# Performance work log

Hardware: AMD Instinct MI355X
Metric: run time of the kernel (lower is better)

The kernel has to match this reference:

```python
import jax, jax.numpy as jnp
import numpy as np

SHUFFLE_G = 8
NUM_HEADS = 8
EPS = 1e-12


def setup_inputs() -> dict:
    key = jax.random.key(0)
    ks = jax.random.split(key, 7)
    b, dim, t, h, w = 2, 64, 10, 128, 128
    c3 = dim * 3
    return {
        "x": jax.random.normal(ks[0], (b, dim, t, h, w), jnp.float32),
        "W1": jax.random.normal(ks[1], (c3, dim), jnp.float32) * 0.05,            # 1x1x1 conv
        "Wdw": jax.random.normal(ks[2], (c3, 1, 1, 3, 3), jnp.float32) * 0.1,     # depthwise (1,3,3) conv
        "W_lin": jax.random.normal(ks[3], (t * SHUFFLE_G, t * SHUFFLE_G), jnp.float32) * 0.05,
        "b_lin": jax.random.normal(ks[4], (t * SHUFFLE_G,), jnp.float32) * 0.01,
        "temperature": jnp.ones((NUM_HEADS, 1, 1), jnp.float32),
        "W_out": jax.random.normal(ks[5], (dim, dim), jnp.float32) * 0.05,        # 1x1x1 conv
    }


def _l2norm(v):
    n = jnp.sqrt(jnp.sum(v * v, axis=-1, keepdims=True))
    return v / jnp.maximum(n, EPS)


def reference(x, W1, Wdw, W_lin, b_lin, temperature, W_out):
    b, c, t, h, w = x.shape
    c3 = 3 * c
    heads = NUM_HEADS
    # 1x1x1 pointwise conv (no bias)
    y = jnp.einsum('oc,bcthw->bothw', W1, x)
    # depthwise (1,3,3) conv, padding (0,1,1)
    y = jax.lax.conv_general_dilated(
        y, Wdw, window_strides=(1, 1, 1),
        padding=((0, 0), (1, 1), (1, 1)),
        dimension_numbers=('NCDHW', 'OIDHW', 'NCDHW'),
        feature_group_count=c3)
    # shuffle: b (c1 c2) t h w -> b c2 h w (c1 t), c1 = SHUFFLE_G
    c1, c2 = SHUFFLE_G, c3 // SHUFFLE_G
    y = y.reshape(b, c1, c2, t, h, w).transpose(0, 2, 4, 5, 1, 3).reshape(b, c2, h, w, c1 * t)
    # linear mixing along (c1 t)
    y = jnp.einsum('bchwi,oi->bchwo', y, W_lin) + b_lin
    # unshuffle: b c2 h w (c1 t) -> b (c2 c1 t) h w
    y = y.reshape(b, c2, h, w, c1, t).transpose(0, 1, 4, 5, 2, 3).reshape(b, c3 * t, h, w)
    # split qkv along channel
    q, k, v = jnp.split(y, 3, axis=1)  # each [b, c*t, h, w]
    ct, hw = (c // heads) * t, h * w
    q = q.reshape(b, heads, ct, hw)
    k = k.reshape(b, heads, ct, hw)
    v = v.reshape(b, heads, ct, hw)
    q = _l2norm(q)
    k = _l2norm(k)
    attn = jnp.einsum('bhcd,bhed->bhce', q, k) * temperature  # [b, heads, ct, ct]
    attn = jax.nn.softmax(attn, axis=-1)
    out = jnp.einsum('bhce,bhed->bhcd', attn, v)  # [b, heads, ct, hw]
    out = out.reshape(b, c, t, h, w)
    out = jnp.einsum('oc,bcthw->bothw', W_out, out)
    return out
```

## Files before the change

### kernel.cpp

```cpp
#include <hip/hip_runtime.h>
#include <hip/hip_bf16.h>

#define C_  64
#define C3_ 192
#define T_  10
#define H_  128
#define W_  128
#define HW_ 16384
#define THW_ 163840
#define NH_ 8
#define C2_ 24
#define TG_ 80

typedef __hip_bfloat16 bf16;
typedef __attribute__((ext_vector_type(8))) short bf16x8;
typedef __attribute__((ext_vector_type(4))) float f32x4;

__device__ __forceinline__ float bf2f(bf16 v) { return __bfloat162float(v); }

__device__ __forceinline__ ushort f2bf_s(float f) {
  bf16 h = __float2bfloat16(f);
  union { bf16 b; ushort s; } u; u.b = h; return u.s;
}

__device__ __forceinline__ ushort4 pack4(f32x4 a) {
  ushort4 p;
  p.x = f2bf_s(a[0]); p.y = f2bf_s(a[1]); p.z = f2bf_s(a[2]); p.w = f2bf_s(a[3]);
  return p;
}

__device__ __forceinline__ uint pack2lo(uint x, uint y) { return (x & 0xffffu) | (y << 16); }
__device__ __forceinline__ uint pack2hi(uint x, uint y) { return (x >> 16) | (y & 0xffff0000u); }

__global__ __launch_bounds__(256) void kprep(
    const float* __restrict__ W1, const float* __restrict__ W_lin,
    const float* __restrict__ W_out,
    bf16* __restrict__ W1bf, bf16* __restrict__ Wlinbf, bf16* __restrict__ Woutbf) {
  const int idx = blockIdx.x * 256 + threadIdx.x;
  if (idx < 12288) {
    W1bf[idx] = __float2bfloat16(W1[idx]);
  } else if (idx < 12288 + 7680) {
    const int i = idx - 12288;
    const int row = i / 96, col = i - row * 96;
    Wlinbf[i] = __float2bfloat16(col < 80 ? W_lin[row * 80 + col] : 0.f);
  } else if (idx < 12288 + 7680 + 4096) {
    const int i = idx - 12288 - 7680;
    Woutbf[i] = __float2bfloat16(W_out[i]);
  }
}

#define K1_TPB 4
__global__ __launch_bounds__(256) void k1_mfma(
    const float* __restrict__ x, const bf16* __restrict__ W1bf,
    bf16* __restrict__ y1ws) {
  __shared__ __align__(16) float xs[2][64 * 128];
  const int tid = threadIdx.x;
  const int lane = tid & 63, wv = tid >> 6;
  const int lr = lane & 15, lg = lane >> 4;
  const int mh = blockIdx.y;
  const int b = blockIdx.z;
  const float* xb = x + (size_t)b * C_ * THW_;
  bf16* y1 = y1ws + (size_t)b * C3_ * THW_;
  const int tile0 = blockIdx.x * K1_TPB;

  const int ro = lane >> 5, colo = (lane & 31) * 4;
  auto STAGE = [&](int buf, int tIdx) {
    const int n0 = tIdx * 128;
#pragma unroll
    for (int i = 0; i < 8; ++i) {
      const int row = wv * 16 + i * 2;
      const float* gsrc = xb + (size_t)(row + ro) * THW_ + n0 + colo;
      __builtin_amdgcn_global_load_lds(
          (const __attribute__((address_space(1))) void*)gsrc,
          (__attribute__((address_space(3))) void*)&xs[buf][row * 128],
          16, 0, 0);
    }
  };

  STAGE(0, tile0);

  bf16x8 wf[6][2];
#pragma unroll
  for (int mt = 0; mt < 6; ++mt)
#pragma unroll
    for (int c = 0; c < 2; ++c) {
      const int row = mh * 96 + mt * 16 + lr;
      wf[mt][c] = *reinterpret_cast<const bf16x8*>(W1bf + row * 64 + c * 32 + lg * 8);
    }
  __syncthreads();

  int buf = 0;
  for (int t = 0; t < K1_TPB; ++t) {
    if (t + 1 < K1_TPB) STAGE(buf ^ 1, tile0 + t + 1);
    const int n0 = (tile0 + t) * 128;
#pragma unroll
    for (int nt = 0; nt < 2; ++nt) {
      const int col = wv * 32 + nt * 16 + lr;
      bf16x8 xa[2];
#pragma unroll
      for (int c = 0; c < 2; ++c) {
        const float* base = &xs[buf][(c * 32 + lg * 8) * 128 + col];
        bf16x8 f;
#pragma unroll
        for (int e = 0; e < 8; ++e) f[e] = f2bf_s(base[e * 128]);
        xa[c] = f;
      }
      f32x4 acc[6];
#pragma unroll
      for (int mt = 0; mt < 6; ++mt) acc[mt] = (f32x4){0.f, 0.f, 0.f, 0.f};
#pragma unroll
      for (int c = 0; c < 2; ++c)
#pragma unroll
        for (int mt = 0; mt < 6; ++mt)
          acc[mt] = __builtin_amdgcn_mfma_f32_16x16x32_bf16(xa[c], wf[mt][c], acc[mt], 0, 0, 0);
      const int nb = n0 + wv * 32 + nt * 16 + lg * 4;
#pragma unroll
      for (int mt = 0; mt < 6; ++mt) {
        const int o = mh * 96 + mt * 16 + lr;
        *reinterpret_cast<ushort4*>(y1 + (size_t)o * THW_ + nb) = pack4(acc[mt]);
      }
    }
    __syncthreads();
    buf ^= 1;
  }
}

__global__ __launch_bounds__(256) void k2_dw(
    const bf16* __restrict__ y1ws, const float* __restrict__ Wdw,
    bf16* __restrict__ y2ws) {
  __shared__ float tile[34][132];
  const int tid = threadIdx.x;
  const int blk = blockIdx.x;
  const int b = blockIdx.y;
  const bf16* y1 = y1ws + (size_t)b * C3_ * THW_;
  bf16* y2 = y2ws + (size_t)b * C3_ * THW_;
  const int hs = (blk & 3) * 32;
  const int rest = blk >> 2;
  const int t = rest % T_;
  const int o = rest / T_;
  const bf16* src = y1 + ((size_t)o * T_ + t) * HW_;

  if (tid < 68) {
    const int r = tid >> 1, side = tid & 1;
    tile[r][side ? 129 : 0] = 0.f;
  }
  {
    const int rr = tid >> 5, c4 = (tid & 31) * 4;
#pragma unroll
    for (int p = 0; p < 5; ++p) {
      const int r = p * 8 + rr;
      if (r < 34) {
        const int hh = hs - 1 + r;
        float e0 = 0.f, e1 = 0.f, e2 = 0.f, e3 = 0.f;
        if (hh >= 0 && hh < H_) {
          uint2 raw = *reinterpret_cast<const uint2*>(src + hh * W_ + c4);
          e0 = __uint_as_float(raw.x << 16);
          e1 = __uint_as_float(raw.x & 0xffff0000u);
          e2 = __uint_as_float(raw.y << 16);
          e3 = __uint_as_float(raw.y & 0xffff0000u);
        }
        tile[r][1 + c4]     = e0;
        tile[r][1 + c4 + 1] = e1;
        tile[r][1 + c4 + 2] = e2;
        tile[r][1 + c4 + 3] = e3;
      }
    }
  }
  __syncthreads();

  float kk[9];
#pragma unroll
  for (int i = 0; i < 9; ++i) kk[i] = Wdw[o * 9 + i];

  bf16* dst = y2 + ((size_t)o * T_ + t) * HW_;
  const int w = tid & 127;
  const int r0 = (tid >> 7) * 16;

  float a[3][3];
#pragma unroll
  for (int ky = 0; ky < 3; ++ky)
#pragma unroll
    for (int kx = 0; kx < 3; ++kx) a[ky][kx] = tile[r0 + ky][w + kx];

#pragma unroll
  for (int q = 0; q < 16; ++q) {
    float acc = 0.f;
#pragma unroll
    for (int ky = 0; ky < 3; ++ky)
#pragma unroll
      for (int kx = 0; kx < 3; ++kx)
        acc = fmaf(kk[ky * 3 + kx], a[ky][kx], acc);
    dst[(hs + r0 + q) * W_ + w] = __float2bfloat16(acc);
    if (q < 15) {
#pragma unroll
      for (int kx = 0; kx < 3; ++kx) {
        a[0][kx] = a[1][kx];
        a[1][kx] = a[2][kx];
        a[2][kx] = tile[r0 + q + 3][w + kx];
      }
    }
  }
}

#define K3_NKC 13
#define K3_STRIDE 208
__global__ __launch_bounds__(256) void k3_mfma(
    const bf16* __restrict__ y2ws, const bf16* __restrict__ Wlinbf,
    const float* __restrict__ b_lin, bf16* __restrict__ zws,
    float* __restrict__ ssqws) {
  __shared__ __align__(16) char lds[256 * K3_STRIDE];
  const int tid = threadIdx.x;
  const int s0 = blockIdx.x * 256;
  const int c2 = blockIdx.y;
  const int b = blockIdx.z;
  const bf16* y2 = y2ws + (size_t)b * C3_ * THW_;
  bf16* z = zws + (size_t)b * C3_ * THW_;
  float* ssq = ssqws + b * 1280;

  {
    auto stage_block = [&](int kc, int cg) {
      uint rr[8][4];
#pragma unroll
      for (int e = 0; e < 8; ++e) {
        const int k = kc * 8 + e;
        const int c1 = (k * 205) >> 11;
        const int tt = k - c1 * 10;
        uint4 raw = *reinterpret_cast<const uint4*>(
            y2 + ((size_t)((c1 * C2_ + c2) * T_ + tt)) * HW_ + s0 + cg * 8);
        rr[e][0] = raw.x; rr[e][1] = raw.y; rr[e][2] = raw.z; rr[e][3] = raw.w;
      }
#pragma unroll
      for (int j = 0; j < 8; ++j) {
        const int d = j >> 1;
        uint4 o;
        if (j & 1) {
          o.x = pack2hi(rr[0][d], rr[1][d]); o.y = pack2hi(rr[2][d], rr[3][d]);
          o.z = pack2hi(rr[4][d], rr[5][d]); o.w = pack2hi(rr[6][d], rr[7][d]);
        } else {
          o.x = pack2lo(rr[0][d], rr[1][d]); o.y = pack2lo(rr[2][d], rr[3][d]);
          o.z = pack2lo(rr[4][d], rr[5][d]); o.w = pack2lo(rr[6][d], rr[7][d]);
        }
        const int col = cg * 8 + j;
        const int r = (kc + col) % K3_NKC;
        *reinterpret_cast<uint4*>(lds + col * K3_STRIDE + r * 16) = o;
      }
    };
    stage_block(tid >> 5, tid & 31);
    if ((tid & 3) == 0) {
      const int q = tid >> 2;
      stage_block(8 + (q >> 5), q & 31);
    }
    const int col = tid;
    const uint4 zero4 = {0, 0, 0, 0};
    *reinterpret_cast<uint4*>(lds + col * K3_STRIDE + ((10 + col) % K3_NKC) * 16) = zero4;
    *reinterpret_cast<uint4*>(lds + col * K3_STRIDE + ((11 + col) % K3_NKC) * 16) = zero4;
  }
  __syncthreads();

  const int lane = tid & 63, wv = tid >> 6;
  const int lr = lane & 15, lg = lane >> 4;

  bf16x8 wf[5][3];
#pragma unroll
  for (int mt = 0; mt < 5; ++mt)
#pragma unroll
    for (int c = 0; c < 3; ++c)
      wf[mt][c] = *reinterpret_cast<const bf16x8*>(
          Wlinbf + (mt * 16 + lr) * 96 + c * 32 + lg * 8);
  float bias[5];
#pragma unroll
  for (int mt = 0; mt < 5; ++mt) bias[mt] = b_lin[mt * 16 + lr];

  float sqp[5] = {0.f, 0.f, 0.f, 0.f, 0.f};

  for (int nt = 0; nt < 4; ++nt) {
    const int col = wv * 64 + nt * 16 + lr;
    bf16x8 xa[3];
#pragma unroll
    for (int c = 0; c < 3; ++c) {
      const int kc = c * 4 + lg;
      xa[c] = *reinterpret_cast<const bf16x8*>(
          lds + col * K3_STRIDE + ((kc + col) % K3_NKC) * 16);
    }
    f32x4 acc[5];
#pragma unroll
    for (int mt = 0; mt < 5; ++mt)
      acc[mt] = (f32x4){bias[mt], bias[mt], bias[mt], bias[mt]};
#pragma unroll
    for (int c = 0; c < 3; ++c)
#pragma unroll
      for (int mt = 0; mt < 5; ++mt)
        acc[mt] = __builtin_amdgcn_mfma_f32_16x16x32_bf16(xa[c], wf[mt][c], acc[mt], 0, 0, 0);
    const int sb = s0 + wv * 64 + nt * 16 + lg * 4;
#pragma unroll
    for (int mt = 0; mt < 5; ++mt) {
      const int u = c2 * TG_ + mt * 16 + lr;
      *reinterpret_cast<ushort4*>(z + (size_t)u * HW_ + sb) = pack4(acc[mt]);
#pragma unroll
      for (int j = 0; j < 4; ++j)
        sqp[mt] = fmaf(acc[mt][j], acc[mt][j], sqp[mt]);
    }
  }

  if (c2 < 16) {
#pragma unroll
    for (int mt = 0; mt < 5; ++mt) {
      float v = sqp[mt];
      v += __shfl_xor(v, 16);
      v += __shfl_xor(v, 32);
      if (lane < 16)
        atomicAdd(&ssq[c2 * TG_ + mt * 16 + lane], v);
    }
  }
}

__global__ __launch_bounds__(256) void k5_mfma(
    const bf16* __restrict__ zws, float* __restrict__ Gpartws) {
  __shared__ __align__(16) float gbuf[2][TG_ * TG_];
  const int chunk = blockIdx.x, h = blockIdx.y, b = blockIdx.z;
  const bf16* z = zws + (size_t)b * C3_ * THW_;
  float* Gpart = Gpartws + (size_t)b * 1638400;
  const int tid = threadIdx.x;
  const int lane = tid & 63, wv = tid >> 6;
  const int lr = lane & 15, lg = lane >> 4;

  const bf16* qbase = z + (size_t)(h * TG_) * HW_;
  const bf16* kbase = z + (size_t)((8 + h) * TG_) * HW_;

  f32x4 acc[5][5];
#pragma unroll
  for (int a = 0; a < 5; ++a)
#pragma unroll
    for (int b2 = 0; b2 < 5; ++b2) acc[a][b2] = (f32x4){0.f, 0.f, 0.f, 0.f};

  const int s0 = chunk * 512 + wv * 128;
  for (int s = s0; s < s0 + 128; s += 32) {
    bf16x8 qa[5], kb[5];
#pragma unroll
    for (int a = 0; a < 5; ++a)
      qa[a] = *reinterpret_cast<const bf16x8*>(qbase + (size_t)(a * 16 + lr) * HW_ + s + lg * 8);
#pragma unroll
    for (int a = 0; a < 5; ++a)
      kb[a] = *reinterpret_cast<const bf16x8*>(kbase + (size_t)(a * 16 + lr) * HW_ + s + lg * 8);
#pragma unroll
    for (int a = 0; a < 5; ++a)
#pragma unroll
      for (int b2 = 0; b2 < 5; ++b2)
        acc[a][b2] = __builtin_amdgcn_mfma_f32_16x16x32_bf16(qa[a], kb[b2], acc[a][b2], 0, 0, 0);
  }

  if (wv == 1 || wv == 3) {
    float* dst = gbuf[wv >> 1];
#pragma unroll
    for (int a = 0; a < 5; ++a)
#pragma unroll
      for (int b2 = 0; b2 < 5; ++b2)
#pragma unroll
        for (int j = 0; j < 4; ++j)
          dst[(a * 16 + lg * 4 + j) * TG_ + b2 * 16 + lr] = acc[a][b2][j];
  }
  __syncthreads();
  if (wv == 0 || wv == 2) {
    const float* srcb = gbuf[wv >> 1];
#pragma unroll
    for (int a = 0; a < 5; ++a)
#pragma unroll
      for (int b2 = 0; b2 < 5; ++b2)
#pragma unroll
        for (int j = 0; j < 4; ++j)
          acc[a][b2][j] += srcb[(a * 16 + lg * 4 + j) * TG_ + b2 * 16 + lr];
  }
  __syncthreads();
  if (wv == 2) {
#pragma unroll
    for (int a = 0; a < 5; ++a)
#pragma unroll
      for (int b2 = 0; b2 < 5; ++b2)
#pragma unroll
        for (int j = 0; j < 4; ++j)
          gbuf[0][(a * 16 + lg * 4 + j) * TG_ + b2 * 16 + lr] = acc[a][b2][j];
  }
  __syncthreads();
  if (wv == 0) {
    float* gp = Gpart + ((size_t)chunk * 8 + h) * TG_ * TG_;
#pragma unroll
    for (int a = 0; a < 5; ++a)
#pragma unroll
      for (int b2 = 0; b2 < 5; ++b2)
#pragma unroll
        for (int j = 0; j < 4; ++j) {
          const int i = a * 16 + lg * 4 + j, jj = b2 * 16 + lr;
          gp[i * TG_ + jj] = acc[a][b2][j] + gbuf[0][i * TG_ + jj];
        }
  }
}

__global__ __launch_bounds__(128) void k6_softmax(
    const float* __restrict__ Gpartws, const float* __restrict__ ssqws,
    const float* __restrict__ temp, bf16* __restrict__ attnbfws) {
  __shared__ float red[128];
  __shared__ float smax, ssum;
  const int b = blockIdx.y;
  const float* Gpart = Gpartws + (size_t)b * 1638400;
  const float* ssq = ssqws + b * 1280;
  bf16* attnbf = attnbfws + (size_t)b * NH_ * TG_ * 96;
  int h = blockIdx.x / TG_, i = blockIdx.x % TG_;
  int j = threadIdx.x;
  float logit = -1e30f;
  if (j < TG_) {
    float g = 0.f;
    for (int c = 0; c < 32; ++c)
      g += Gpart[(((size_t)c * 8 + h) * TG_ + i) * TG_ + j];
    float nq = ssq[h * TG_ + i];
    float nk = ssq[(8 + h) * TG_ + j];
    float sq = 1.f / fmaxf(sqrtf(nq), 1e-12f);
    float sk = 1.f / fmaxf(sqrtf(nk), 1e-12f);
    logit = g * sq * sk * temp[h];
  }
  red[j] = logit;
  __syncthreads();
  if (j == 0) {
    float m = -1e30f;
    for (int x2 = 0; x2 < TG_; ++x2) m = fmaxf(m, red[x2]);
    smax = m;
  }
  __syncthreads();
  float e = (j < TG_) ? expf(logit - smax) : 0.f;
  red[j] = e;
  __syncthreads();
  if (j == 0) {
    float s = 0.f;
    for (int x2 = 0; x2 < TG_; ++x2) s += red[x2];
    ssum = s;
  }
  __syncthreads();
  if (j < 96)
    attnbf[((size_t)h * TG_ + i) * 96 + j] =
        __float2bfloat16(j < TG_ ? e / ssum : 0.f);
}

__global__ __launch_bounds__(256) void k7a_mfma(
    const bf16* __restrict__ zws, const bf16* __restrict__ attnbfws,
    bf16* __restrict__ att_outws) {
  __shared__ __align__(16) char lds[256 * K3_STRIDE];
  const int tid = threadIdx.x;
  const int s0 = blockIdx.x * 256;
  const int h = blockIdx.y;
  const int b = blockIdx.z;
  const bf16* z = zws + (size_t)b * C3_ * THW_;
  const bf16* attnbf = attnbfws + (size_t)b * NH_ * TG_ * 96;
  bf16* att_out = att_outws + (size_t)b * NH_ * TG_ * HW_;
  const int voff = (16 + h) * TG_;

  {
    auto stage_block = [&](int kc, int cg) {
      uint rr[8][4];
#pragma unroll
      for (int e = 0; e < 8; ++e) {
        uint4 raw = *reinterpret_cast<const uint4*>(
            z + (size_t)(voff + kc * 8 + e) * HW_ + s0 + cg * 8);
        rr[e][0] = raw.x; rr[e][1] = raw.y; rr[e][2] = raw.z; rr[e][3] = raw.w;
      }
#pragma unroll
      for (int j = 0; j < 8; ++j) {
        const int d = j >> 1;
        uint4 o;
        if (j & 1) {
          o.x = pack2hi(rr[0][d], rr[1][d]); o.y = pack2hi(rr[2][d], rr[3][d]);
          o.z = pack2hi(rr[4][d], rr[5][d]); o.w = pack2hi(rr[6][d], rr[7][d]);
        } else {
          o.x = pack2lo(rr[0][d], rr[1][d]); o.y = pack2lo(rr[2][d], rr[3][d]);
          o.z = pack2lo(rr[4][d], rr[5][d]); o.w = pack2lo(rr[6][d], rr[7][d]);
        }
        const int col = cg * 8 + j;
        const int r = (kc + col) % K3_NKC;
        *reinterpret_cast<uint4*>(lds + col * K3_STRIDE + r * 16) = o;
      }
    };
    stage_block(tid >> 5, tid & 31);
    if ((tid & 3) == 0) {
      const int q = tid >> 2;
      stage_block(8 + (q >> 5), q & 31);
    }
    const int col = tid;
    const uint4 zero4 = {0, 0, 0, 0};
    *reinterpret_cast<uint4*>(lds + col * K3_STRIDE + ((10 + col) % K3_NKC) * 16) = zero4;
    *reinterpret_cast<uint4*>(lds + col * K3_STRIDE + ((11 + col) % K3_NKC) * 16) = zero4;
  }
  __syncthreads();

  const int lane = tid & 63, wv = tid >> 6;
  const int lr = lane & 15, lg = lane >> 4;

  bf16x8 wf[5][3];
#pragma unroll
  for (int mt = 0; mt < 5; ++mt)
#pragma unroll
    for (int c = 0; c < 3; ++c)
      wf[mt][c] = *reinterpret_cast<const bf16x8*>(
          attnbf + ((size_t)h * TG_ + mt * 16 + lr) * 96 + c * 32 + lg * 8);

  for (int nt = 0; nt < 4; ++nt) {
    const int col = wv * 64 + nt * 16 + lr;
    bf16x8 xa[3];
#pragma unroll
    for (int c = 0; c < 3; ++c) {
      const int kc = c * 4 + lg;
      xa[c] = *reinterpret_cast<const bf16x8*>(
          lds + col * K3_STRIDE + ((kc + col) % K3_NKC) * 16);
    }
    f32x4 acc[5];
#pragma unroll
    for (int mt = 0; mt < 5; ++mt) acc[mt] = (f32x4){0.f, 0.f, 0.f, 0.f};
#pragma unroll
    for (int c = 0; c < 3; ++c)
#pragma unroll
      for (int mt = 0; mt < 5; ++mt)
        acc[mt] = __builtin_amdgcn_mfma_f32_16x16x32_bf16(xa[c], wf[mt][c], acc[mt], 0, 0, 0);
    const int sb = s0 + wv * 64 + nt * 16 + lg * 4;
#pragma unroll
    for (int mt = 0; mt < 5; ++mt) {
      const int u = h * TG_ + mt * 16 + lr;
      *reinterpret_cast<ushort4*>(att_out + (size_t)u * HW_ + sb) = pack4(acc[mt]);
    }
  }
}

#define K1_NKC 10
#define K1_STRIDE 160
__global__ __launch_bounds__(256) void k7b_mfma(
    const bf16* __restrict__ att_outws, const bf16* __restrict__ Woutbf,
    float* __restrict__ out) {
  __shared__ __align__(16) char lds[256 * K1_STRIDE];
  const int tid = threadIdx.x;
  const int n0 = blockIdx.x * 256;
  const int b = blockIdx.y;
  const bf16* att_out = att_outws + (size_t)b * NH_ * TG_ * HW_;
  float* outb = out + (size_t)b * C_ * THW_;
  const int t = n0 >> 14;
  const int sb0 = n0 & (HW_ - 1);

  {
    const int kc = tid >> 5, cg = tid & 31;
    uint rr[8][4];
#pragma unroll
    for (int e = 0; e < 8; ++e) {
      const int row = kc * TG_ + e * T_ + t;
      uint4 raw = *reinterpret_cast<const uint4*>(
          att_out + (size_t)row * HW_ + sb0 + cg * 8);
      rr[e][0] = raw.x; rr[e][1] = raw.y; rr[e][2] = raw.z; rr[e][3] = raw.w;
    }
#pragma unroll
    for (int j = 0; j < 8; ++j) {
      const int d = j >> 1;
      uint4 o;
      if (j & 1) {
        o.x = pack2hi(rr[0][d], rr[1][d]); o.y = pack2hi(rr[2][d], rr[3][d]);
        o.z = pack2hi(rr[4][d], rr[5][d]); o.w = pack2hi(rr[6][d], rr[7][d]);
      } else {
        o.x = pack2lo(rr[0][d], rr[1][d]); o.y = pack2lo(rr[2][d], rr[3][d]);
        o.z = pack2lo(rr[4][d], rr[5][d]); o.w = pack2lo(rr[6][d], rr[7][d]);
      }
      const int col = cg * 8 + j;
      const int r = (kc + col) % K1_NKC;
      *reinterpret_cast<uint4*>(lds + col * K1_STRIDE + r * 16) = o;
    }
  }
  __syncthreads();

  const int lane = tid & 63, wv = tid >> 6;
  const int lr = lane & 15, lg = lane >> 4;

  bf16x8 wf[4][2];
#pragma unroll
  for (int mt = 0; mt < 4; ++mt)
#pragma unroll
    for (int c = 0; c < 2; ++c)
      wf[mt][c] = *reinterpret_cast<const bf16x8*>(
          Woutbf + (mt * 16 + lr) * 64 + c * 32 + lg * 8);

  for (int nt = 0; nt < 4; ++nt) {
    const int col = wv * 64 + nt * 16 + lr;
    bf16x8 xa[2];
#pragma unroll
    for (int c = 0; c < 2; ++c) {
      const int kc = c * 4 + lg;
      xa[c] = *reinterpret_cast<const bf16x8*>(
          lds + col * K1_STRIDE + ((kc + col) % K1_NKC) * 16);
    }
    f32x4 acc[4];
#pragma unroll
    for (int mt = 0; mt < 4; ++mt) acc[mt] = (f32x4){0.f, 0.f, 0.f, 0.f};
#pragma unroll
    for (int c = 0; c < 2; ++c)
#pragma unroll
      for (int mt = 0; mt < 4; ++mt)
        acc[mt] = __builtin_amdgcn_mfma_f32_16x16x32_bf16(xa[c], wf[mt][c], acc[mt], 0, 0, 0);
    const int nb = n0 + wv * 64 + nt * 16 + lg * 4;
#pragma unroll
    for (int mt = 0; mt < 4; ++mt) {
      const int o = mt * 16 + lr;
      *reinterpret_cast<float4*>(outb + (size_t)o * THW_ + nb) =
          (float4){acc[mt][0], acc[mt][1], acc[mt][2], acc[mt][3]};
    }
  }
}

extern "C" void kernel_launch(void* const* d_in, const int* in_sizes, int n_in,
                              void* d_out, int out_size, void* d_ws, size_t ws_size,
                              hipStream_t stream) {
  const float* x    = (const float*)d_in[0];
  const float* W1   = (const float*)d_in[1];
  const float* Wdw  = (const float*)d_in[2];
  const float* Wlin = (const float*)d_in[3];
  const float* blin = (const float*)d_in[4];
  const float* temp = (const float*)d_in[5];
  const float* Wout = (const float*)d_in[6];
  float* out = (float*)d_out;

  const size_t NY = (size_t)C3_ * THW_;
  char* ws = (char*)d_ws;
  bf16* y1z = (bf16*)ws;
  bf16* y2  = (bf16*)(ws + 4 * NY);
  char* E   = ws + 8 * NY;
  float* Gpart  = (float*)E;
  bf16* attnbf  = (bf16*)(E + 13107200);
  bf16* att_out = (bf16*)(E + 13352960);
  float* ssq    = (float*)(E + 55296000);
  bf16* W1bf    = (bf16*)(E + 55306240);
  bf16* Wlinbf  = (bf16*)(E + 55330816);
  bf16* Woutbf  = (bf16*)(E + 55346176);

  kprep<<<94, 256, 0, stream>>>(W1, Wlin, Wout, W1bf, Wlinbf, Woutbf);
  hipMemsetAsync(ssq, 0, 2 * 1280 * sizeof(float), stream);
  k1_mfma<<<dim3(THW_ / 128 / K1_TPB, 2, 2), 256, 0, stream>>>(x, W1bf, y1z);
  k2_dw<<<dim3(C3_ * T_ * 4, 2), 256, 0, stream>>>(y1z, Wdw, y2);
  k3_mfma<<<dim3(HW_ / 256, C2_, 2), 256, 0, stream>>>(y2, Wlinbf, blin, y1z, ssq);
  k5_mfma<<<dim3(32, NH_, 2), 256, 0, stream>>>(y1z, Gpart);
  k6_softmax<<<dim3(NH_ * TG_, 2), 128, 0, stream>>>(Gpart, ssq, temp, attnbf);
  k7a_mfma<<<dim3(HW_ / 256, NH_, 2), 256, 0, stream>>>(y1z, attnbf, att_out);
  k7b_mfma<<<dim3(THW_ / 256, 2), 256, 0, stream>>>(att_out, Woutbf, out);
}
```

Baseline: 284.4 us.

## Process four tiles per block with register-prefetched loads in k3, k7a, k7b

k3, k7a and k7b now loop over four 256-column tiles per block instead of one, cutting their grid sizes by four. The global loads for the next tile are issued into registers before the current tile's MFMA work, so memory latency overlaps compute. This spreads the weight-fragment loads and setup over more tiles. The cost is fewer blocks (less parallelism and occupancy slack), a second __syncthreads per tile, and higher register pressure from the double register buffers.

```diff
diff --git a/kernel.cpp b/kernel.cpp
--- a/kernel.cpp
+++ b/kernel.cpp
@@ -31,6 +31,25 @@
 
 __device__ __forceinline__ uint pack2lo(uint x, uint y) { return (x & 0xffffu) | (y << 16); }
 __device__ __forceinline__ uint pack2hi(uint x, uint y) { return (x >> 16) | (y & 0xffff0000u); }
+
+__device__ __forceinline__ void twrite(char* lds, int stride, int nkc,
+                                       uint r[8][4], int kc, int cg) {
+#pragma unroll
+  for (int j = 0; j < 8; ++j) {
+    const int d = j >> 1;
+    uint4 o;
+    if (j & 1) {
+      o.x = pack2hi(r[0][d], r[1][d]); o.y = pack2hi(r[2][d], r[3][d]);
+      o.z = pack2hi(r[4][d], r[5][d]); o.w = pack2hi(r[6][d], r[7][d]);
+    } else {
+      o.x = pack2lo(r[0][d], r[1][d]); o.y = pack2lo(r[2][d], r[3][d]);
+      o.z = pack2lo(r[4][d], r[5][d]); o.w = pack2lo(r[6][d], r[7][d]);
+    }
+    const int col = cg * 8 + j;
+    const int rr = (kc + col) % nkc;
+    *reinterpret_cast<uint4*>(lds + col * stride + rr * 16) = o;
+  }
+}
 
 __global__ __launch_bounds__(256) void kprep(
     const float* __restrict__ W1, const float* __restrict__ W_lin,
@@ -204,61 +223,49 @@
 
 #define K3_NKC 13
 #define K3_STRIDE 208
+#define K3_TPB 4
 __global__ __launch_bounds__(256) void k3_mfma(
     const bf16* __restrict__ y2ws, const bf16* __restrict__ Wlinbf,
     const float* __restrict__ b_lin, bf16* __restrict__ zws,
     float* __restrict__ ssqws) {
   __shared__ __align__(16) char lds[256 * K3_STRIDE];
   const int tid = threadIdx.x;
-  const int s0 = blockIdx.x * 256;
+  const int tile0 = blockIdx.x * K3_TPB;
   const int c2 = blockIdx.y;
   const int b = blockIdx.z;
   const bf16* y2 = y2ws + (size_t)b * C3_ * THW_;
   bf16* z = zws + (size_t)b * C3_ * THW_;
   float* ssq = ssqws + b * 1280;
 
+  const int lane = tid & 63, wv = tid >> 6;
+  const int lr = lane & 15, lg = lane >> 4;
+
+  const int kcA = tid >> 5, cgA = tid & 31;
+  const bool hasB = (tid & 3) == 0;
+  const int qB = tid >> 2;
+  const int kcB = 8 + (qB >> 5), cgB = qB & 31;
+
+  uint rrA[8][4], rrB[8][4];
+  auto LOAD = [&](int s0, uint r[8][4], int kc, int cg) {
+#pragma unroll
+    for (int e = 0; e < 8; ++e) {
+      const int k = kc * 8 + e;
+      const int c1 = (k * 205) >> 11;
+      const int tt = k - c1 * 10;
+      uint4 raw = *reinterpret_cast<const uint4*>(
+          y2 + ((size_t)((c1 * C2_ + c2) * T_ + tt)) * HW_ + s0 + cg * 8);
+      r[e][0] = raw.x; r[e][1] = raw.y; r[e][2] = raw.z; r[e][3] = raw.w;
+    }
+  };
+
+  LOAD(tile0 * 256, rrA, kcA, cgA);
+  if (hasB) LOAD(tile0 * 256, rrB, kcB, cgB);
   {
-    auto stage_block = [&](int kc, int cg) {
-      uint rr[8][4];
-#pragma unroll
-      for (int e = 0; e < 8; ++e) {
-        const int k = kc * 8 + e;
-        const int c1 = (k * 205) >> 11;
-        const int tt = k - c1 * 10;
-        uint4 raw = *reinterpret_cast<const uint4*>(
-            y2 + ((size_t)((c1 * C2_ + c2) * T_ + tt)) * HW_ + s0 + cg * 8);
-        rr[e][0] = raw.x; rr[e][1] = raw.y; rr[e][2] = raw.z; rr[e][3] = raw.w;
-      }
-#pragma unroll
-      for (int j = 0; j < 8; ++j) {
-        const int d = j >> 1;
-        uint4 o;
-        if (j & 1) {
-          o.x = pack2hi(rr[0][d], rr[1][d]); o.y = pack2hi(rr[2][d], rr[3][d]);
-          o.z = pack2hi(rr[4][d], rr[5][d]); o.w = pack2hi(rr[6][d], rr[7][d]);
-        } else {
-          o.x = pack2lo(rr[0][d], rr[1][d]); o.y = pack2lo(rr[2][d], rr[3][d]);
-          o.z = pack2lo(rr[4][d], rr[5][d]); o.w = pack2lo(rr[6][d], rr[7][d]);
-        }
-        const int col = cg * 8 + j;
-        const int r = (kc + col) % K3_NKC;
-        *reinterpret_cast<uint4*>(lds + col * K3_STRIDE + r * 16) = o;
-      }
-    };
-    stage_block(tid >> 5, tid & 31);
-    if ((tid & 3) == 0) {
-      const int q = tid >> 2;
-      stage_block(8 + (q >> 5), q & 31);
-    }
     const int col = tid;
     const uint4 zero4 = {0, 0, 0, 0};
     *reinterpret_cast<uint4*>(lds + col * K3_STRIDE + ((10 + col) % K3_NKC) * 16) = zero4;
     *reinterpret_cast<uint4*>(lds + col * K3_STRIDE + ((11 + col) % K3_NKC) * 16) = zero4;
   }
-  __syncthreads();
-
-  const int lane = tid & 63, wv = tid >> 6;
-  const int lr = lane & 15, lg = lane >> 4;
 
   bf16x8 wf[5][3];
 #pragma unroll
@@ -273,33 +280,46 @@
 
   float sqp[5] = {0.f, 0.f, 0.f, 0.f, 0.f};
 
-  for (int nt = 0; nt < 4; ++nt) {
-    const int col = wv * 64 + nt * 16 + lr;
-    bf16x8 xa[3];
-#pragma unroll
-    for (int c = 0; c < 3; ++c) {
-      const int kc = c * 4 + lg;
-      xa[c] = *reinterpret_cast<const bf16x8*>(
-          lds + col * K3_STRIDE + ((kc + col) % K3_NKC) * 16);
-    }
-    f32x4 acc[5];
-#pragma unroll
-    for (int mt = 0; mt < 5; ++mt)
-      acc[mt] = (f32x4){bias[mt], bias[mt], bias[mt], bias[mt]};
-#pragma unroll
-    for (int c = 0; c < 3; ++c)
+#pragma unroll
+  for (int t = 0; t < K3_TPB; ++t) {
+    const int s0 = (tile0 + t) * 256;
+    twrite(lds, K3_STRIDE, K3_NKC, rrA, kcA, cgA);
+    if (hasB) twrite(lds, K3_STRIDE, K3_NKC, rrB, kcB, cgB);
+    if (t + 1 < K3_TPB) {
+      LOAD(s0 + 256, rrA, kcA, cgA);
+      if (hasB) LOAD(s0 + 256, rrB, kcB, cgB);
+    }
+    __syncthreads();
+
+    for (int nt = 0; nt < 4; ++nt) {
+      const int col = wv * 64 + nt * 16 + lr;
+      bf16x8 xa[3];
+#pragma unroll
+      for (int c = 0; c < 3; ++c) {
+        const int kc = c * 4 + lg;
+        xa[c] = *reinterpret_cast<const bf16x8*>(
+            lds + col * K3_STRIDE + ((kc + col) % K3_NKC) * 16);
+      }
+      f32x4 acc[5];
 #pragma unroll
       for (int mt = 0; mt < 5; ++mt)
-        acc[mt] = __builtin_amdgcn_mfma_f32_16x16x32_bf16(xa[c], wf[mt][c], acc[mt], 0, 0, 0);
-    const int sb = s0 + wv * 64 + nt * 16 + lg * 4;
-#pragma unroll
-    for (int mt = 0; mt < 5; ++mt) {
-      const int u = c2 * TG_ + mt * 16 + lr;
-      *reinterpret_cast<ushort4*>(z + (size_t)u * HW_ + sb) = pack4(acc[mt]);
-#pragma unroll
-      for (int j = 0; j < 4; ++j)
-        sqp[mt] = fmaf(acc[mt][j], acc[mt][j], sqp[mt]);
-    }
+        acc[mt] = (f32x4){bias[mt], bias[mt], bias[mt], bias[mt]};
+#pragma unroll
+      for (int c = 0; c < 3; ++c)
+#pragma unroll
+        for (int mt = 0; mt < 5; ++mt)
+          acc[mt] = __builtin_amdgcn_mfma_f32_16x16x32_bf16(xa[c], wf[mt][c], acc[mt], 0, 0, 0);
+      const int sb = s0 + wv * 64 + nt * 16 + lg * 4;
+#pragma unroll
+      for (int mt = 0; mt < 5; ++mt) {
+        const int u = c2 * TG_ + mt * 16 + lr;
+        *reinterpret_cast<ushort4*>(z + (size_t)u * HW_ + sb) = pack4(acc[mt]);
+#pragma unroll
+        for (int j = 0; j < 4; ++j)
+          sqp[mt] = fmaf(acc[mt][j], acc[mt][j], sqp[mt]);
+      }
+    }
+    __syncthreads();
   }
 
   if (c2 < 16) {
@@ -439,12 +459,13 @@
         __float2bfloat16(j < TG_ ? e / ssum : 0.f);
 }
 
+#define K7A_TPB 4
 __global__ __launch_bounds__(256) void k7a_mfma(
     const bf16* __restrict__ zws, const bf16* __restrict__ attnbfws,
     bf16* __restrict__ att_outws) {
   __shared__ __align__(16) char lds[256 * K3_STRIDE];
   const int tid = threadIdx.x;
-  const int s0 = blockIdx.x * 256;
+  const int tile0 = blockIdx.x * K7A_TPB;
   const int h = blockIdx.y;
   const int b = blockIdx.z;
   const bf16* z = zws + (size_t)b * C3_ * THW_;
@@ -452,45 +473,32 @@
   bf16* att_out = att_outws + (size_t)b * NH_ * TG_ * HW_;
   const int voff = (16 + h) * TG_;
 
+  const int lane = tid & 63, wv = tid >> 6;
+  const int lr = lane & 15, lg = lane >> 4;
+
+  const int kcA = tid >> 5, cgA = tid & 31;
+  const bool hasB = (tid & 3) == 0;
+  const int qB = tid >> 2;
+  const int kcB = 8 + (qB >> 5), cgB = qB & 31;
+
+  uint rrA[8][4], rrB[8][4];
+  auto LOAD = [&](int s0, uint r[8][4], int kc, int cg) {
+#pragma unroll
+    for (int e = 0; e < 8; ++e) {
+      uint4 raw = *reinterpret_cast<const uint4*>(
+          z + (size_t)(voff + kc * 8 + e) * HW_ + s0 + cg * 8);
+      r[e][0] = raw.x; r[e][1] = raw.y; r[e][2] = raw.z; r[e][3] = raw.w;
+    }
+  };
+
+  LOAD(tile0 * 256, rrA, kcA, cgA);
+  if (hasB) LOAD(tile0 * 256, rrB, kcB, cgB);
   {
-    auto stage_block = [&](int kc, int cg) {
-      uint rr[8][4];
-#pragma unroll
-      for (int e = 0; e < 8; ++e) {
-        uint4 raw = *reinterpret_cast<const uint4*>(
-            z + (size_t)(voff + kc * 8 + e) * HW_ + s0 + cg * 8);
-        rr[e][0] = raw.x; rr[e][1] = raw.y; rr[e][2] = raw.z; rr[e][3] = raw.w;
-      }
-#pragma unroll
-      for (int j = 0; j < 8; ++j) {
-        const int d = j >> 1;
-        uint4 o;
-        if (j & 1) {
-          o.x = pack2hi(rr[0][d], rr[1][d]); o.y = pack2hi(rr[2][d], rr[3][d]);
-          o.z = pack2hi(rr[4][d], rr[5][d]); o.w = pack2hi(rr[6][d], rr[7][d]);
-        } else {
-          o.x = pack2lo(rr[0][d], rr[1][d]); o.y = pack2lo(rr[2][d], rr[3][d]);
-          o.z = pack2lo(rr[4][d], rr[5][d]); o.w = pack2lo(rr[6][d], rr[7][d]);
-        }
-        const int col = cg * 8 + j;
-        const int r = (kc + col) % K3_NKC;
-        *reinterpret_cast<uint4*>(lds + col * K3_STRIDE + r * 16) = o;
-      }
-    };
-    stage_block(tid >> 5, tid & 31);
-    if ((tid & 3) == 0) {
-      const int q = tid >> 2;
-      stage_block(8 + (q >> 5), q & 31);
-    }
     const int col = tid;
     const uint4 zero4 = {0, 0, 0, 0};
     *reinterpret_cast<uint4*>(lds + col * K3_STRIDE + ((10 + col) % K3_NKC) * 16) = zero4;
     *reinterpret_cast<uint4*>(lds + col * K3_STRIDE + ((11 + col) % K3_NKC) * 16) = zero4;
   }
-  __syncthreads();
-
-  const int lane = tid & 63, wv = tid >> 6;
-  const int lr = lane & 15, lg = lane >> 4;
 
   bf16x8 wf[5][3];
 #pragma unroll
@@ -500,76 +508,75 @@
       wf[mt][c] = *reinterpret_cast<const bf16x8*>(
           attnbf + ((size_t)h * TG_ + mt * 16 + lr) * 96 + c * 32 + lg * 8);
 
-  for (int nt = 0; nt < 4; ++nt) {
-    const int col = wv * 64 + nt * 16 + lr;
-    bf16x8 xa[3];
-#pragma unroll
-    for (int c = 0; c < 3; ++c) {
-      const int kc = c * 4 + lg;
-      xa[c] = *reinterpret_cast<const bf16x8*>(
-          lds + col * K3_STRIDE + ((kc + col) % K3_NKC) * 16);
-    }
-    f32x4 acc[5];
-#pragma unroll
-    for (int mt = 0; mt < 5; ++mt) acc[mt] = (f32x4){0.f, 0.f, 0.f, 0.f};
-#pragma unroll
-    for (int c = 0; c < 3; ++c)
-#pragma unroll
-      for (int mt = 0; mt < 5; ++mt)
-        acc[mt] = __builtin_amdgcn_mfma_f32_16x16x32_bf16(xa[c], wf[mt][c], acc[mt], 0, 0, 0);
-    const int sb = s0 + wv * 64 + nt * 16 + lg * 4;
-#pragma unroll
-    for (int mt = 0; mt < 5; ++mt) {
-      const int u = h * TG_ + mt * 16 + lr;
-      *reinterpret_cast<ushort4*>(att_out + (size_t)u * HW_ + sb) = pack4(acc[mt]);
-    }
+#pragma unroll
+  for (int t = 0; t < K7A_TPB; ++t) {
+    const int s0 = (tile0 + t) * 256;
+    twrite(lds, K3_STRIDE, K3_NKC, rrA, kcA, cgA);
+    if (hasB) twrite(lds, K3_STRIDE, K3_NKC, rrB, kcB, cgB);
+    if (t + 1 < K7A_TPB) {
+      LOAD(s0 + 256, rrA, kcA, cgA);
+      if (hasB) LOAD(s0 + 256, rrB, kcB, cgB);
+    }
+    __syncthreads();
+
+    for (int nt = 0; nt < 4; ++nt) {
+      const int col = wv * 64 + nt * 16 + lr;
+      bf16x8 xa[3];
+#pragma unroll
+      for (int c = 0; c < 3; ++c) {
+        const int kc = c * 4 + lg;
+        xa[c] = *reinterpret_cast<const bf16x8*>(
+            lds + col * K3_STRIDE + ((kc + col) % K3_NKC) * 16);
+      }
+      f32x4 acc[5];
+#pragma unroll
+      for (int mt = 0; mt < 5; ++mt) acc[mt] = (f32x4){0.f, 0.f, 0.f, 0.f};
+#pragma unroll
+      for (int c = 0; c < 3; ++c)
+#pragma unroll
+        for (int mt = 0; mt < 5; ++mt)
+          acc[mt] = __builtin_amdgcn_mfma_f32_16x16x32_bf16(xa[c], wf[mt][c], acc[mt], 0, 0, 0);
+      const int sb = s0 + wv * 64 + nt * 16 + lg * 4;
+#pragma unroll
+      for (int mt = 0; mt < 5; ++mt) {
+        const int u = h * TG_ + mt * 16 + lr;
+        *reinterpret_cast<ushort4*>(att_out + (size_t)u * HW_ + sb) = pack4(acc[mt]);
+      }
+    }
+    __syncthreads();
   }
 }
 
 #define K1_NKC 10
 #define K1_STRIDE 160
+#define K7B_TPB 4
 __global__ __launch_bounds__(256) void k7b_mfma(
     const bf16* __restrict__ att_outws, const bf16* __restrict__ Woutbf,
     float* __restrict__ out) {
   __shared__ __align__(16) char lds[256 * K1_STRIDE];
   const int tid = threadIdx.x;
-  const int n0 = blockIdx.x * 256;
+  const int tile0 = blockIdx.x * K7B_TPB;
   const int b = blockIdx.y;
   const bf16* att_out = att_outws + (size_t)b * NH_ * TG_ * HW_;
   float* outb = out + (size_t)b * C_ * THW_;
-  const int t = n0 >> 14;
-  const int sb0 = n0 & (HW_ - 1);
-
-  {
-    const int kc = tid >> 5, cg = tid & 31;
-    uint rr[8][4];
-#pragma unroll
-    for (int e = 0; e < 8; ++e) {
-      const int row = kc * TG_ + e * T_ + t;
-      uint4 raw = *reinterpret_cast<const uint4*>(
-          att_out + (size_t)row * HW_ + sb0 + cg * 8);
-      rr[e][0] = raw.x; rr[e][1] = raw.y; rr[e][2] = raw.z; rr[e][3] = raw.w;
-    }
-#pragma unroll
-    for (int j = 0; j < 8; ++j) {
-      const int d = j >> 1;
-      uint4 o;
-      if (j & 1) {
-        o.x = pack2hi(rr[0][d], rr[1][d]); o.y = pack2hi(rr[2][d], rr[3][d]);
-        o.z = pack2hi(rr[4][d], rr[5][d]); o.w = pack2hi(rr[6][d], rr[7][d]);
-      } else {
-        o.x = pack2lo(rr[0][d], rr[1][d]); o.y = pack2lo(rr[2][d], rr[3][d]);
-        o.z = pack2lo(rr[4][d], rr[5][d]); o.w = pack2lo(rr[6][d], rr[7][d]);
-      }
-      const int col = cg * 8 + j;
-      const int r = (kc + col) % K1_NKC;
-      *reinterpret_cast<uint4*>(lds + col * K1_STRIDE + r * 16) = o;
-    }
-  }
-  __syncthreads();
-
+  const int t_ = tile0 >> 6;
   const int lane = tid & 63, wv = tid >> 6;
   const int lr = lane & 15, lg = lane >> 4;
+
+  const int kcA = tid >> 5, cgA = tid & 31;
+  uint rrA[8][4];
+  auto LOAD = [&](int tile, uint r[8][4]) {
+    const int sb0 = (tile * 256) & (HW_ - 1);
+#pragma unroll
+    for (int e = 0; e < 8; ++e) {
+      const int row = kcA * TG_ + e * T_ + t_;
+      uint4 raw = *reinterpret_cast<const uint4*>(
+          att_out + (size_t)row * HW_ + sb0 + cgA * 8);
+      r[e][0] = raw.x; r[e][1] = raw.y; r[e][2] = raw.z; r[e][3] = raw.w;
+    }
+  };
+
+  LOAD(tile0, rrA);
 
   bf16x8 wf[4][2];
 #pragma unroll
@@ -579,30 +586,39 @@
       wf[mt][c] = *reinterpret_cast<const bf16x8*>(
           Woutbf + (mt * 16 + lr) * 64 + c * 32 + lg * 8);
 
-  for (int nt = 0; nt < 4; ++nt) {
-    const int col = wv * 64 + nt * 16 + lr;
-    bf16x8 xa[2];
-#pragma unroll
-    for (int c = 0; c < 2; ++c) {
-      const int kc = c * 4 + lg;
-      xa[c] = *reinterpret_cast<const bf16x8*>(
-          lds + col * K1_STRIDE + ((kc + col) % K1_NKC) * 16);
-    }
-    f32x4 acc[4];
-#pragma unroll
-    for (int mt = 0; mt < 4; ++mt) acc[mt] = (f32x4){0.f, 0.f, 0.f, 0.f};
-#pragma unroll
-    for (int c = 0; c < 2; ++c)
-#pragma unroll
-      for (int mt = 0; mt < 4; ++mt)
-        acc[mt] = __builtin_amdgcn_mfma_f32_16x16x32_bf16(xa[c], wf[mt][c], acc[mt], 0, 0, 0);
-    const int nb = n0 + wv * 64 + nt * 16 + lg * 4;
-#pragma unroll
-    for (int mt = 0; mt < 4; ++mt) {
-      const int o = mt * 16 + lr;
-      *reinterpret_cast<float4*>(outb + (size_t)o * THW_ + nb) =
-          (float4){acc[mt][0], acc[mt][1], acc[mt][2], acc[mt][3]};
-    }
+#pragma unroll
+  for (int t = 0; t < K7B_TPB; ++t) {
+    const int n0 = (tile0 + t) * 256;
+    twrite(lds, K1_STRIDE, K1_NKC, rrA, kcA, cgA);
+    if (t + 1 < K7B_TPB) LOAD(tile0 + t + 1, rrA);
+    __syncthreads();
+
+    for (int nt = 0; nt < 4; ++nt) {
+      const int col = wv * 64 + nt * 16 + lr;
+      bf16x8 xa[2];
+#pragma unroll
+      for (int c = 0; c < 2; ++c) {
+        const int kc = c * 4 + lg;
+        xa[c] = *reinterpret_cast<const bf16x8*>(
+            lds + col * K1_STRIDE + ((kc + col) % K1_NKC) * 16);
+      }
+      f32x4 acc[4];
+#pragma unroll
+      for (int mt = 0; mt < 4; ++mt) acc[mt] = (f32x4){0.f, 0.f, 0.f, 0.f};
+#pragma unroll
+      for (int c = 0; c < 2; ++c)
+#pragma unroll
+        for (int mt = 0; mt < 4; ++mt)
+          acc[mt] = __builtin_amdgcn_mfma_f32_16x16x32_bf16(xa[c], wf[mt][c], acc[mt], 0, 0, 0);
+      const int nb = n0 + wv * 64 + nt * 16 + lg * 4;
+#pragma unroll
+      for (int mt = 0; mt < 4; ++mt) {
+        const int o = mt * 16 + lr;
+        *reinterpret_cast<float4*>(outb + (size_t)o * THW_ + nb) =
+            (float4){acc[mt][0], acc[mt][1], acc[mt][2], acc[mt][3]};
+      }
+    }
+    __syncthreads();
   }
 }
 
@@ -635,9 +651,9 @@
   hipMemsetAsync(ssq, 0, 2 * 1280 * sizeof(float), stream);
   k1_mfma<<<dim3(THW_ / 128 / K1_TPB, 2, 2), 256, 0, stream>>>(x, W1bf, y1z);
   k2_dw<<<dim3(C3_ * T_ * 4, 2), 256, 0, stream>>>(y1z, Wdw, y2);
-  k3_mfma<<<dim3(HW_ / 256, C2_, 2), 256, 0, stream>>>(y2, Wlinbf, blin, y1z, ssq);
+  k3_mfma<<<dim3(HW_ / 256 / K3_TPB, C2_, 2), 256, 0, stream>>>(y2, Wlinbf, blin, y1z, ssq);
   k5_mfma<<<dim3(32, NH_, 2), 256, 0, stream>>>(y1z, Gpart);
   k6_softmax<<<dim3(NH_ * TG_, 2), 128, 0, stream>>>(Gpart, ssq, temp, attnbf);
-  k7a_mfma<<<dim3(HW_ / 256, NH_, 2), 256, 0, stream>>>(y1z, attnbf, att_out);
-  k7b_mfma<<<dim3(THW_ / 256, 2), 256, 0, stream>>>(att_out, Woutbf, out);
-}
+  k7a_mfma<<<dim3(HW_ / 256 / K7A_TPB, NH_, 2), 256, 0, stream>>>(y1z, attnbf, att_out);
+  k7b_mfma<<<dim3(THW_ / 256 / K7B_TPB, 2), 256, 0, stream>>>(att_out, Woutbf, out);
+}
```

Measured after the change: 284.9 us. About the same (+0.2%).
